# Kernel tuning notes

Hardware: AMD Instinct MI355X
Metric: run time of the kernel (lower is better)

## Reference

```python
import jax, jax.numpy as jnp
import numpy as np

F, H, K, T, IT, S = 128, 128, 768, 4, 2, 57  # feat, hidden, max_child, edge types, iters, num_sem


def setup_inputs() -> dict:
    key = jax.random.key(0)
    ks = jax.random.split(key, 12)

    def w(k, shape):
        fan = shape[0] if len(shape) == 2 else shape[1]
        return jax.random.normal(k, shape, jnp.float32) * fan ** -0.5

    return {
        "parent_feature": jax.random.normal(ks[0], (1, F), jnp.float32),
        "W_parent": w(ks[1], (F, H * K)), "b_parent": jnp.zeros((H * K,), jnp.float32),
        "W_exists": w(ks[2], (H, 1)), "b_exists": jnp.zeros((1,), jnp.float32),
        "W_edge_lat": w(ks[3], (2 * H, H)), "b_edge_lat": jnp.zeros((H,), jnp.float32),
        "W_edge_ex": w(ks[4], (T, H)), "b_edge_ex": jnp.zeros((T,), jnp.float32),
        "W_ne": w(ks[5], (IT, 2 * H, H)), "b_ne": jnp.zeros((IT, H), jnp.float32),
        "W_child": w(ks[6], (H * (IT + 1), H)), "b_child": jnp.zeros((H,), jnp.float32),
        "W_sem": w(ks[7], (H, S)), "b_sem": jnp.zeros((S,), jnp.float32),
        "W_child2": w(ks[8], (H, F)), "b_child2": jnp.zeros((F,), jnp.float32),
    }


def reference(parent_feature, W_parent, b_parent, W_exists, b_exists,
              W_edge_lat, b_edge_lat, W_edge_ex, b_edge_ex,
              W_ne, b_ne, W_child, b_child, W_sem, b_sem, W_child2, b_child2):
    # parent -> K child latents
    x = jax.nn.relu(parent_feature @ W_parent + b_parent)  # [1, K*H]
    cf = x.reshape(1, K, H)                                 # child feats
    exists_logits = cf @ W_exists + b_exists                # [1, K, 1]

    # pairwise edge latents [1, K, K, 2H] -> [1, K, K, H]
    pair0 = jnp.concatenate([
        jnp.broadcast_to(cf[:, :, None, :], (1, K, K, H)),
        jnp.broadcast_to(cf[:, None, :, :], (1, K, K, H))], axis=3)
    elat = jax.nn.relu(pair0 @ W_edge_lat + b_edge_lat)
    edge_logits = jnp.einsum('bijh,th->bijt', elat, W_edge_ex) + b_edge_ex  # [1,K,K,T]

    # fixed edge set: existing edges between existing nodes (dense mask form)
    exists = exists_logits[0, :, 0] > 0                     # [K]
    emask = jnp.any(edge_logits[0] > 0, axis=-1) & exists[:, None] & exists[None, :]
    any_edge = jnp.any(emask)

    feats = [cf]
    for i in range(IT):
        c = cf[0]                                           # [K, H]
        pair = jnp.concatenate([
            jnp.broadcast_to(c[:, None, :], (K, K, H)),
            jnp.broadcast_to(c[None, :, :], (K, K, H))], axis=2)
        msg = jax.nn.relu(pair @ W_ne[i] + b_ne[i])         # [K, K, H], >= 0
        msg = jnp.where(emask[:, :, None], msg, 0.0)
        # scatter_max with zeros-initialized out == max over masked neighbors (msg >= 0)
        new_cf = msg.max(axis=1)[None]                      # [1, K, H]
        cf = jnp.where(any_edge, new_cf, cf)                # no edges -> feats unchanged
        feats.append(cf)

    h = jnp.concatenate(feats, axis=2).reshape(K, H * (IT + 1))
    h = jax.nn.relu(h @ W_child + b_child)                  # [K, H]
    sem_logits = (h @ W_sem + b_sem).reshape(1, K, S)
    child_out = jax.nn.relu(h @ W_child2 + b_child2).reshape(1, K, F)
    return child_out, sem_logits, exists_logits, edge_logits
```

## Files before the change

kernel.cpp:

```cpp
#include <hip/hip_runtime.h>
#include <hip/hip_bf16.h>


#define NK 768
#define NH 128
#define NCF 98304

typedef float v2f __attribute__((ext_vector_type(2)));

__global__ __launch_bounds__(256) void k_parent(const float* __restrict__ pf,
    const float* __restrict__ Wp, const float* __restrict__ bp,
    const float* __restrict__ Wexi, const float* __restrict__ bexi,
    float* __restrict__ cf0, float* __restrict__ exO, unsigned int* __restrict__ flag)
{
    __shared__ float s_pf[128];
    __shared__ float4 s_part[8][32];
    int t = threadIdx.x;
    if (t < 128) s_pf[t] = pf[t];
    if (blockIdx.x == 0 && t == 0) *flag = 0u;
    __syncthreads();
    int c = t & 31, g = t >> 5;
    int col4 = blockIdx.x * 32 + c;
    const float4* W4 = (const float4*)Wp;
    float4 acc = make_float4(0.f, 0.f, 0.f, 0.f);
    #pragma unroll
    for (int q = 0; q < 16; ++q) {
        int f = g * 16 + q;
        float4 w = W4[(size_t)f * 24576 + col4];
        float p = s_pf[f];
        acc.x = fmaf(p, w.x, acc.x);
        acc.y = fmaf(p, w.y, acc.y);
        acc.z = fmaf(p, w.z, acc.z);
        acc.w = fmaf(p, w.w, acc.w);
    }
    s_part[g][c] = acc;
    __syncthreads();
    if (t < 32) {
        float4 r = s_part[0][t];
        #pragma unroll
        for (int q = 1; q < 8; ++q) {
            float4 p = s_part[q][t];
            r.x += p.x; r.y += p.y; r.z += p.z; r.w += p.w;
        }
        float4 bi = ((const float4*)bp)[col4];
        r.x = fmaxf(r.x + bi.x, 0.f);
        r.y = fmaxf(r.y + bi.y, 0.f);
        r.z = fmaxf(r.z + bi.z, 0.f);
        r.w = fmaxf(r.w + bi.w, 0.f);
        ((float4*)cf0)[col4] = r;
        float4 w = ((const float4*)Wexi)[t];
        float dot = r.x * w.x + r.y * w.y + r.z * w.z + r.w * w.w;
        dot += __shfl_xor(dot, 16);
        dot += __shfl_xor(dot, 8);
        dot += __shfl_xor(dot, 4);
        dot += __shfl_xor(dot, 2);
        dot += __shfl_xor(dot, 1);
        if (t == 0) exO[blockIdx.x] = dot + bexi[0];
    }
}

__global__ __launch_bounds__(512) void k_dualmm(const float* __restrict__ src,
    const float* __restrict__ Wel, float* __restrict__ A, float* __restrict__ BT,
    const float* __restrict__ Wne, float* __restrict__ A0, float* __restrict__ B0)
{
    __shared__ float s_cf[4][128];
    __shared__ float s_bt[128][4];
    int t = threadIdx.x;
    int k0 = blockIdx.x * 4;
    int set = blockIdx.y;
    s_cf[t >> 7][t & 127] = src[k0 * 128 + t];
    __syncthreads();
    int h = t & 127, sub = (t >> 7) & 1, half = t >> 8;
    const float* W = (set ? Wne : Wel) + half * 16384;
    const float* c0 = &s_cf[sub * 2][0];
    const float* c1 = &s_cf[sub * 2 + 1][0];
    float a0 = 0.f, a1 = 0.f;
    #pragma unroll 8
    for (int r = 0; r < 128; ++r) {
        float w = W[r * 128 + h];
        a0 = fmaf(c0[r], w, a0);
        a1 = fmaf(c1[r], w, a1);
    }
    if (half == 0) {
        float* D = set ? A0 : A;
        D[(k0 + sub * 2) * 128 + h] = a0;
        D[(k0 + sub * 2 + 1) * 128 + h] = a1;
    } else if (set) {
        B0[(k0 + sub * 2) * 128 + h] = a0;
        B0[(k0 + sub * 2 + 1) * 128 + h] = a1;
    } else {
        s_bt[h][sub * 2] = a0;
        s_bt[h][sub * 2 + 1] = a1;
    }
    __syncthreads();
    if (set == 0 && t < 128)
        *(float4*)(BT + (size_t)t * NK + k0) = *(const float4*)&s_bt[t][0];
}

__global__ __launch_bounds__(256) void k_edge(const float* __restrict__ A,
    const float* __restrict__ BT, const float* __restrict__ b_lat,
    const float* __restrict__ Wex, const float* __restrict__ bex,
    const float* __restrict__ exO, float* __restrict__ edge_out,
    unsigned char* __restrict__ mask, unsigned int* __restrict__ flag)
{
    __shared__ float4 s_A[128];
    __shared__ float4 s_W[128];
    __shared__ float s_B[2][16][256];
    __shared__ float s_exi[4];
    __shared__ unsigned int s_any;
    int t = threadIdx.x;
    int i0 = blockIdx.x * 4;
    int j = blockIdx.y * 256 + t;
    float exj = exO[j];
    if (t < 128) {
        float bl = b_lat[t];
        s_A[t] = make_float4(A[(i0 + 0) * 128 + t] + bl, A[(i0 + 1) * 128 + t] + bl,
                             A[(i0 + 2) * 128 + t] + bl, A[(i0 + 3) * 128 + t] + bl);
        s_W[t] = make_float4(Wex[t], Wex[128 + t], Wex[256 + t], Wex[384 + t]);
    }
    if (t < 4) s_exi[t] = exO[i0 + t];
    if (t == 0) s_any = 0u;
    const float4* BT4 = (const float4*)BT;
    int row = t >> 6, col = t & 63;
    {
        #pragma unroll
        for (int k = 0; k < 4; ++k)
            *(float4*)&s_B[0][row + k * 4][col * 4] =
                BT4[(size_t)(row + k * 4) * 192 + blockIdx.y * 64 + col];
    }
    __syncthreads();
    v2f l01[4] = {}, l23[4] = {};
    for (int c = 0; c < 8; ++c) {
        float4 r0, r1, r2, r3;
        if (c < 7) {
            size_t base = (size_t)((c + 1) * 16 + row) * 192 + blockIdx.y * 64 + col;
            r0 = BT4[base];
            r1 = BT4[base + 4 * 192];
            r2 = BT4[base + 8 * 192];
            r3 = BT4[base + 12 * 192];
        }
        int buf = c & 1;
        #pragma unroll
        for (int hh = 0; hh < 16; ++hh) {
            float bv = s_B[buf][hh][t];
            float4 av = s_A[c * 16 + hh];
            float4 wv = s_W[c * 16 + hh];
            v2f e01 = __builtin_elementwise_max((v2f){av.x + bv, av.y + bv}, (v2f){0.f, 0.f});
            v2f e23 = __builtin_elementwise_max((v2f){av.z + bv, av.w + bv}, (v2f){0.f, 0.f});
            l01[0] += e01 * wv.x; l01[1] += e01 * wv.y;
            l01[2] += e01 * wv.z; l01[3] += e01 * wv.w;
            l23[0] += e23 * wv.x; l23[1] += e23 * wv.y;
            l23[2] += e23 * wv.z; l23[3] += e23 * wv.w;
        }
        if (c < 7) {
            int nb = (c + 1) & 1;
            *(float4*)&s_B[nb][row + 0][col * 4] = r0;
            *(float4*)&s_B[nb][row + 4][col * 4] = r1;
            *(float4*)&s_B[nb][row + 8][col * 4] = r2;
            *(float4*)&s_B[nb][row + 12][col * 4] = r3;
        }
        __syncthreads();
    }
    float b0 = bex[0], b1 = bex[1], b2 = bex[2], b3 = bex[3];
    bool ej = exj > 0.f;
    float4 v0 = make_float4(l01[0].x + b0, l01[1].x + b1, l01[2].x + b2, l01[3].x + b3);
    float4 v1 = make_float4(l01[0].y + b0, l01[1].y + b1, l01[2].y + b2, l01[3].y + b3);
    float4 v2 = make_float4(l23[0].x + b0, l23[1].x + b1, l23[2].x + b2, l23[3].x + b3);
    float4 v3 = make_float4(l23[0].y + b0, l23[1].y + b1, l23[2].y + b2, l23[3].y + b3);
    ((float4*)edge_out)[(size_t)(i0 + 0) * NK + j] = v0;
    ((float4*)edge_out)[(size_t)(i0 + 1) * NK + j] = v1;
    ((float4*)edge_out)[(size_t)(i0 + 2) * NK + j] = v2;
    ((float4*)edge_out)[(size_t)(i0 + 3) * NK + j] = v3;
    bool m0 = ((v0.x > 0.f) | (v0.y > 0.f) | (v0.z > 0.f) | (v0.w > 0.f)) && ej && (s_exi[0] > 0.f);
    bool m1 = ((v1.x > 0.f) | (v1.y > 0.f) | (v1.z > 0.f) | (v1.w > 0.f)) && ej && (s_exi[1] > 0.f);
    bool m2 = ((v2.x > 0.f) | (v2.y > 0.f) | (v2.z > 0.f) | (v2.w > 0.f)) && ej && (s_exi[2] > 0.f);
    bool m3 = ((v3.x > 0.f) | (v3.y > 0.f) | (v3.z > 0.f) | (v3.w > 0.f)) && ej && (s_exi[3] > 0.f);
    mask[(i0 + 0) * NK + j] = m0 ? (unsigned char)1 : (unsigned char)0;
    mask[(i0 + 1) * NK + j] = m1 ? (unsigned char)1 : (unsigned char)0;
    mask[(i0 + 2) * NK + j] = m2 ? (unsigned char)1 : (unsigned char)0;
    mask[(i0 + 3) * NK + j] = m3 ? (unsigned char)1 : (unsigned char)0;
    unsigned long long bal = __ballot((m0 | m1 | m2 | m3) ? 1 : 0);
    if ((t & 63) == 0 && bal) s_any = 1u;
    __syncthreads();
    if (t == 0 && s_any) *flag = 1u;
}

__global__ __launch_bounds__(256) void k_mm(const float* __restrict__ Bm,
    const unsigned char* __restrict__ mask, float* __restrict__ Mp)
{
    __shared__ float s_B[32][128];
    __shared__ float s_madd[96][8];
    int t = threadIdx.x;
    int i0 = blockIdx.x * 8;
    int j0 = blockIdx.y * 96;
    for (int idx = t; idx < 768; idx += 256) {
        int jj = idx >> 3, i = idx & 7;
        s_madd[jj][i] = mask[(i0 + i) * NK + j0 + jj] ? 0.f : -1e30f;
    }
    int p = t & 63, g = t >> 6;
    v2f M0 = {-1e30f, -1e30f}, M1 = {-1e30f, -1e30f};
    const float4* B4 = (const float4*)Bm;
    for (int c = 0; c < 3; ++c) {
        __syncthreads();
        #pragma unroll
        for (int k = 0; k < 4; ++k) {
            int idx = t + k * 256;
            ((float4*)s_B)[idx] = B4[(size_t)(j0 + c * 32) * 32 + idx];
        }
        __syncthreads();
        #pragma unroll 8
        for (int jj = 0; jj < 32; ++jj) {
            v2f b = *(const v2f*)&s_B[jj][2 * p];
            float m0 = s_madd[c * 32 + jj][2 * g];
            float m1 = s_madd[c * 32 + jj][2 * g + 1];
            M0 = __builtin_elementwise_max(M0, b + (v2f){m0, m0});
            M1 = __builtin_elementwise_max(M1, b + (v2f){m1, m1});
        }
    }
    float* Mb = Mp + (size_t)blockIdx.y * NCF;
    *(v2f*)&Mb[(i0 + 2 * g) * 128 + 2 * p] = M0;
    *(v2f*)&Mb[(i0 + 2 * g + 1) * 128 + 2 * p] = M1;
}

__global__ __launch_bounds__(512) void k_cmb1(const float* __restrict__ Mp,
    const float* __restrict__ A0, const float* __restrict__ bne,
    const float* __restrict__ cf0, const unsigned int* __restrict__ flag,
    float* __restrict__ cf1, const float* __restrict__ Wne1,
    float* __restrict__ A1, float* __restrict__ B1)
{
    __shared__ float s_cf[2][128];
    int t = threadIdx.x;
    int k0 = blockIdx.x * 2;
    unsigned int fl = *flag;
    if (t < 256) {
        int kk = t >> 7, hh = t & 127;
        int g = (k0 + kk) * 128 + hh;
        float M = Mp[g];
        #pragma unroll
        for (int q = 1; q < 8; ++q) M = fmaxf(M, Mp[q * NCF + g]);
        float v = fl ? fmaxf(A0[g] + bne[hh] + M, 0.f) : cf0[g];
        s_cf[kk][hh] = v;
        cf1[g] = v;
    }
    __syncthreads();
    int h = t & 127, kk = (t >> 7) & 1, half = t >> 8;
    const float* W = Wne1 + half * 16384;
    const float* c = &s_cf[kk][0];
    float acc = 0.f;
    #pragma unroll 8
    for (int r = 0; r < 128; ++r)
        acc = fmaf(c[r], W[r * 128 + h], acc);
    float* D = half ? B1 : A1;
    D[(k0 + kk) * 128 + h] = acc;
}

__global__ __launch_bounds__(512) void k_final(const float* __restrict__ cf0,
    const float* __restrict__ cf1, const float* __restrict__ Mp,
    const float* __restrict__ A1, const float* __restrict__ bne1,
    const unsigned int* __restrict__ flag,
    const float* __restrict__ Wc, const float* __restrict__ bc,
    const float* __restrict__ Wsem, const float* __restrict__ bsem,
    const float* __restrict__ W2, const float* __restrict__ b2,
    float* __restrict__ out)
{
    __shared__ float s_f[2][384];
    __shared__ float s_h[2][128];
    __shared__ float s_hp[2][128];
    int t = threadIdx.x;
    int k0 = blockIdx.x * 2;
    unsigned int fl = *flag;
    for (int idx = t; idx < 768; idx += 512) {
        int kk = idx >= 384 ? 1 : 0;
        int c = idx - kk * 384;
        int row = k0 + kk;
        float v;
        if (c < 128) v = cf0[row * 128 + c];
        else if (c < 256) v = cf1[row * 128 + (c - 128)];
        else {
            int hh = c - 256, g = row * 128 + hh;
            float M = Mp[g];
            #pragma unroll
            for (int q = 1; q < 8; ++q) M = fmaxf(M, Mp[q * NCF + g]);
            v = fl ? fmaxf(A1[g] + bne1[hh] + M, 0.f) : cf1[g];
        }
        s_f[kk][c] = v;
    }
    __syncthreads();
    int h = t & 127, rh = (t >> 7) & 1, kg = t >> 8;
    float acc = 0.f;
    {
        const float* f = &s_f[kg][rh * 192];
        const float* Wcp = Wc + rh * 192 * 128;
        #pragma unroll 8
        for (int r = 0; r < 192; ++r)
            acc = fmaf(f[r], Wcp[r * 128 + h], acc);
    }
    if (rh) s_hp[kg][h] = acc;
    __syncthreads();
    if (!rh) s_h[kg][h] = fmaxf(acc + s_hp[kg][h] + bc[h], 0.f);
    __syncthreads();
    float a2 = 0.f;
    {
        const float* hr = &s_h[kg][rh * 64];
        const float* W2p = W2 + rh * 64 * 128;
        #pragma unroll 8
        for (int r = 0; r < 64; ++r)
            a2 = fmaf(hr[r], W2p[r * 128 + h], a2);
    }
    if (rh) s_hp[kg][h] = a2;
    __syncthreads();
    if (!rh) out[(size_t)(k0 + kg) * 128 + h] = fmaxf(a2 + s_hp[kg][h] + b2[h], 0.f);
    if (t < 114) {
        int kk = t / 57, sidx = t - kk * 57;
        float ss = bsem[sidx];
        const float* hr = &s_h[kk][0];
        #pragma unroll 8
        for (int r = 0; r < 128; ++r)
            ss = fmaf(hr[r], Wsem[r * 57 + sidx], ss);
        out[98304 + (size_t)(k0 + kk) * 57 + sidx] = ss;
    }
}

extern "C" void kernel_launch(void* const* d_in, const int* in_sizes, int n_in,
                              void* d_out, int out_size, void* d_ws, size_t ws_size,
                              hipStream_t stream) {
    const float* pf   = (const float*)d_in[0];
    const float* Wp   = (const float*)d_in[1];
    const float* bp   = (const float*)d_in[2];
    const float* Wexi = (const float*)d_in[3];
    const float* bexi = (const float*)d_in[4];
    const float* Wel  = (const float*)d_in[5];
    const float* bel  = (const float*)d_in[6];
    const float* Wee  = (const float*)d_in[7];
    const float* bee  = (const float*)d_in[8];
    const float* Wne  = (const float*)d_in[9];
    const float* bne  = (const float*)d_in[10];
    const float* Wc   = (const float*)d_in[11];
    const float* bc   = (const float*)d_in[12];
    const float* Wsem = (const float*)d_in[13];
    const float* bsem = (const float*)d_in[14];
    const float* W2   = (const float*)d_in[15];
    const float* b2   = (const float*)d_in[16];
    float* out = (float*)d_out;
    float* ws  = (float*)d_ws;
    const int N = NCF;
    float* cf0 = ws;
    float* cf1 = ws + N;
    float* A   = ws + 2 * N;
    float* BT  = ws + 3 * N;
    float* A0  = ws + 4 * N;
    float* B0  = ws + 5 * N;
    float* A1  = ws + 6 * N;
    float* B1  = ws + 7 * N;
    float* Mp  = ws + 8 * N;
    unsigned char* mask = (unsigned char*)(ws + 16 * N);
    unsigned int* flag  = (unsigned int*)(mask + 589824);

    float* out_ex   = out + 142080;
    float* out_edge = out + 142848;

    k_parent<<<768, 256, 0, stream>>>(pf, Wp, bp, Wexi, bexi, cf0, out_ex, flag);
    k_dualmm<<<dim3(192, 2), 512, 0, stream>>>(cf0, Wel, A, BT, Wne, A0, B0);
    k_edge<<<dim3(192, 3), 256, 0, stream>>>(A, BT, bel, Wee, bee, out_ex, out_edge, mask, flag);
    k_mm<<<dim3(96, 8), 256, 0, stream>>>(B0, mask, Mp);
    k_cmb1<<<384, 512, 0, stream>>>(Mp, A0, bne, cf0, flag, cf1, Wne + 32768, A1, B1);
    k_mm<<<dim3(96, 8), 256, 0, stream>>>(B1, mask, Mp);
    k_final<<<384, 512, 0, stream>>>(cf0, cf1, Mp, A1, bne + 128, flag,
                                     Wc, bc, Wsem, bsem, W2, b2, out);
}
```

Measured before the change: 83.45 us.

## Fuse parent projection and dual matmul into a single kernel

Merges the parent-to-child projection kernel and the four small 128x128 projections (edge latent and first node-edge halves) into one kernel. Each block now computes two child rows and immediately multiplies them from shared memory, which removes one launch and the round-trip of cf0 through global memory. In exchange, every block rereads all four 128x128 weight matrices for only two rows, giving less weight reuse than the old four-row tiling, and BT is written with scattered scalar stores.

After: 81.47 us. 1.02x faster.

```diff
diff --git a/kernel.cpp b/kernel.cpp
--- a/kernel.cpp
+++ b/kernel.cpp
@@ -8,93 +8,108 @@
 
 typedef float v2f __attribute__((ext_vector_type(2)));
 
-__global__ __launch_bounds__(256) void k_parent(const float* __restrict__ pf,
+__global__ __launch_bounds__(512) void k_pd(const float* __restrict__ pf,
     const float* __restrict__ Wp, const float* __restrict__ bp,
     const float* __restrict__ Wexi, const float* __restrict__ bexi,
-    float* __restrict__ cf0, float* __restrict__ exO, unsigned int* __restrict__ flag)
+    const float* __restrict__ Wel, const float* __restrict__ Wne,
+    float* __restrict__ cf0g, float* __restrict__ exO,
+    float* __restrict__ A, float* __restrict__ BT,
+    float* __restrict__ A0, float* __restrict__ B0, unsigned int* __restrict__ flag)
 {
     __shared__ float s_pf[128];
-    __shared__ float4 s_part[8][32];
-    int t = threadIdx.x;
+    __shared__ float s_cf0[2][128];
+    __shared__ __align__(16) char s_scr[16384];
+    int t = threadIdx.x;
+    int b = blockIdx.x;
+    int k0 = 2 * b;
     if (t < 128) s_pf[t] = pf[t];
-    if (blockIdx.x == 0 && t == 0) *flag = 0u;
-    __syncthreads();
-    int c = t & 31, g = t >> 5;
-    int col4 = blockIdx.x * 32 + c;
-    const float4* W4 = (const float4*)Wp;
-    float4 acc = make_float4(0.f, 0.f, 0.f, 0.f);
-    #pragma unroll
-    for (int q = 0; q < 16; ++q) {
-        int f = g * 16 + q;
-        float4 w = W4[(size_t)f * 24576 + col4];
-        float p = s_pf[f];
-        acc.x = fmaf(p, w.x, acc.x);
-        acc.y = fmaf(p, w.y, acc.y);
-        acc.z = fmaf(p, w.z, acc.z);
-        acc.w = fmaf(p, w.w, acc.w);
-    }
-    s_part[g][c] = acc;
-    __syncthreads();
-    if (t < 32) {
-        float4 r = s_part[0][t];
-        #pragma unroll
-        for (int q = 1; q < 8; ++q) {
-            float4 p = s_part[q][t];
-            r.x += p.x; r.y += p.y; r.z += p.z; r.w += p.w;
-        }
-        float4 bi = ((const float4*)bp)[col4];
-        r.x = fmaxf(r.x + bi.x, 0.f);
-        r.y = fmaxf(r.y + bi.y, 0.f);
-        r.z = fmaxf(r.z + bi.z, 0.f);
-        r.w = fmaxf(r.w + bi.w, 0.f);
-        ((float4*)cf0)[col4] = r;
-        float4 w = ((const float4*)Wexi)[t];
-        float dot = r.x * w.x + r.y * w.y + r.z * w.z + r.w * w.w;
-        dot += __shfl_xor(dot, 16);
-        dot += __shfl_xor(dot, 8);
-        dot += __shfl_xor(dot, 4);
-        dot += __shfl_xor(dot, 2);
-        dot += __shfl_xor(dot, 1);
-        if (t == 0) exO[blockIdx.x] = dot + bexi[0];
-    }
-}
-
-__global__ __launch_bounds__(512) void k_dualmm(const float* __restrict__ src,
-    const float* __restrict__ Wel, float* __restrict__ A, float* __restrict__ BT,
-    const float* __restrict__ Wne, float* __restrict__ A0, float* __restrict__ B0)
-{
-    __shared__ float s_cf[4][128];
-    __shared__ float s_bt[128][4];
-    int t = threadIdx.x;
-    int k0 = blockIdx.x * 4;
-    int set = blockIdx.y;
-    s_cf[t >> 7][t & 127] = src[k0 * 128 + t];
-    __syncthreads();
-    int h = t & 127, sub = (t >> 7) & 1, half = t >> 8;
-    const float* W = (set ? Wne : Wel) + half * 16384;
-    const float* c0 = &s_cf[sub * 2][0];
-    const float* c1 = &s_cf[sub * 2 + 1][0];
-    float a0 = 0.f, a1 = 0.f;
-    #pragma unroll 8
-    for (int r = 0; r < 128; ++r) {
-        float w = W[r * 128 + h];
-        a0 = fmaf(c0[r], w, a0);
-        a1 = fmaf(c1[r], w, a1);
-    }
-    if (half == 0) {
-        float* D = set ? A0 : A;
-        D[(k0 + sub * 2) * 128 + h] = a0;
-        D[(k0 + sub * 2 + 1) * 128 + h] = a1;
-    } else if (set) {
-        B0[(k0 + sub * 2) * 128 + h] = a0;
-        B0[(k0 + sub * 2 + 1) * 128 + h] = a1;
-    } else {
-        s_bt[h][sub * 2] = a0;
-        s_bt[h][sub * 2 + 1] = a1;
-    }
-    __syncthreads();
-    if (set == 0 && t < 128)
-        *(float4*)(BT + (size_t)t * NK + k0) = *(const float4*)&s_bt[t][0];
+    if (b == 0 && t == 0) *flag = 0u;
+    __syncthreads();
+    {
+        float4* s_part = (float4*)s_scr;
+        int c = t & 63, g = t >> 6;
+        const float4* W4 = (const float4*)Wp;
+        size_t base = (size_t)b * 64 + c;
+        float4 acc = make_float4(0.f, 0.f, 0.f, 0.f);
+        #pragma unroll
+        for (int q = 0; q < 16; ++q) {
+            int f = g * 16 + q;
+            float4 w = W4[(size_t)f * 24576 + base];
+            float p = s_pf[f];
+            acc.x = fmaf(p, w.x, acc.x);
+            acc.y = fmaf(p, w.y, acc.y);
+            acc.z = fmaf(p, w.z, acc.z);
+            acc.w = fmaf(p, w.w, acc.w);
+        }
+        s_part[g * 64 + c] = acc;
+        __syncthreads();
+        if (t < 64) {
+            float4 r = s_part[t];
+            #pragma unroll
+            for (int g2 = 1; g2 < 8; ++g2) {
+                float4 p = s_part[g2 * 64 + t];
+                r.x += p.x; r.y += p.y; r.z += p.z; r.w += p.w;
+            }
+            float4 bi = ((const float4*)bp)[b * 64 + t];
+            r.x = fmaxf(r.x + bi.x, 0.f);
+            r.y = fmaxf(r.y + bi.y, 0.f);
+            r.z = fmaxf(r.z + bi.z, 0.f);
+            r.w = fmaxf(r.w + bi.w, 0.f);
+            int row = t >> 5, h4 = t & 31;
+            *(float4*)&s_cf0[row][h4 * 4] = r;
+            ((float4*)cf0g)[(size_t)b * 64 + t] = r;
+            float4 w = ((const float4*)Wexi)[h4];
+            float dot = r.x * w.x + r.y * w.y + r.z * w.z + r.w * w.w;
+            dot += __shfl_xor(dot, 16);
+            dot += __shfl_xor(dot, 8);
+            dot += __shfl_xor(dot, 4);
+            dot += __shfl_xor(dot, 2);
+            dot += __shfl_xor(dot, 1);
+            if (h4 == 0) exO[k0 + row] = dot + bexi[0];
+        }
+    }
+    __syncthreads();
+    {
+        float4* s_p2 = (float4*)s_scr;
+        int mat = t >> 7, q = (t >> 5) & 3, c = t & 31;
+        const float* W = (mat == 0) ? Wel : (mat == 1) ? (Wel + 16384)
+                       : (mat == 2) ? Wne : (Wne + 16384);
+        float4 a0 = make_float4(0.f, 0.f, 0.f, 0.f);
+        float4 a1 = make_float4(0.f, 0.f, 0.f, 0.f);
+        #pragma unroll 8
+        for (int x = q * 32; x < q * 32 + 32; ++x) {
+            float4 w = *(const float4*)&W[x * 128 + c * 4];
+            float c0 = s_cf0[0][x], c1 = s_cf0[1][x];
+            a0.x = fmaf(c0, w.x, a0.x); a0.y = fmaf(c0, w.y, a0.y);
+            a0.z = fmaf(c0, w.z, a0.z); a0.w = fmaf(c0, w.w, a0.w);
+            a1.x = fmaf(c1, w.x, a1.x); a1.y = fmaf(c1, w.y, a1.y);
+            a1.z = fmaf(c1, w.z, a1.z); a1.w = fmaf(c1, w.w, a1.w);
+        }
+        s_p2[((mat * 4 + q) * 2 + 0) * 32 + c] = a0;
+        s_p2[((mat * 4 + q) * 2 + 1) * 32 + c] = a1;
+        __syncthreads();
+        if (t < 256) {
+            int m2 = t >> 6, row = (t >> 5) & 1, c2 = t & 31;
+            float4 r = s_p2[((m2 * 4 + 0) * 2 + row) * 32 + c2];
+            #pragma unroll
+            for (int q2 = 1; q2 < 4; ++q2) {
+                float4 p = s_p2[((m2 * 4 + q2) * 2 + row) * 32 + c2];
+                r.x += p.x; r.y += p.y; r.z += p.z; r.w += p.w;
+            }
+            if (m2 == 0) {
+                ((float4*)A)[(size_t)(k0 + row) * 32 + c2] = r;
+            } else if (m2 == 1) {
+                BT[(c2 * 4 + 0) * NK + k0 + row] = r.x;
+                BT[(c2 * 4 + 1) * NK + k0 + row] = r.y;
+                BT[(c2 * 4 + 2) * NK + k0 + row] = r.z;
+                BT[(c2 * 4 + 3) * NK + k0 + row] = r.w;
+            } else if (m2 == 2) {
+                ((float4*)A0)[(size_t)(k0 + row) * 32 + c2] = r;
+            } else {
+                ((float4*)B0)[(size_t)(k0 + row) * 32 + c2] = r;
+            }
+        }
+    }
 }
 
 __global__ __launch_bounds__(256) void k_edge(const float* __restrict__ A,
@@ -359,8 +374,8 @@
     float* out_ex   = out + 142080;
     float* out_edge = out + 142848;
 
-    k_parent<<<768, 256, 0, stream>>>(pf, Wp, bp, Wexi, bexi, cf0, out_ex, flag);
-    k_dualmm<<<dim3(192, 2), 512, 0, stream>>>(cf0, Wel, A, BT, Wne, A0, B0);
+    k_pd<<<384, 512, 0, stream>>>(pf, Wp, bp, Wexi, bexi, Wel, Wne,
+                                  cf0, out_ex, A, BT, A0, B0, flag);
     k_edge<<<dim3(192, 3), 256, 0, stream>>>(A, BT, bel, Wee, bee, out_ex, out_edge, mask, flag);
     k_mm<<<dim3(96, 8), 256, 0, stream>>>(B0, mask, Mp);
     k_cmb1<<<384, 512, 0, stream>>>(Mp, A0, bne, cf0, flag, cf1, Wne + 32768, A1, B1);
```
